# Optimization experiments

Measured on AMD Instinct MI355X. Metric: run time of the kernel, lower is better.

Reference implementation:

```python
import jax, jax.numpy as jnp
import numpy as np

# Model config (mirrors Mamba2Block(dim=256) with mamba_ssm defaults)
D_MODEL = 256
EXPAND = 2
D_INNER = D_MODEL * EXPAND          # 512
HEADDIM = D_MODEL * EXPAND // 8     # 64
NHEADS = D_INNER // HEADDIM         # 8
D_STATE = 64
D_CONV = 4
CONV_DIM = D_INNER + 2 * D_STATE    # 640 (ngroups=1)
D_IN_PROJ = 2 * D_INNER + 2 * D_STATE + NHEADS  # 1160
BATCH, SEQLEN = 2, 2048
EPS = 1e-5


def setup_inputs() -> dict:
    key = jax.random.key(0)
    ks = jax.random.split(key, 12)
    s = 0.02
    return {
        "hidden_states": jax.random.normal(ks[0], (BATCH, SEQLEN, D_MODEL), jnp.float32),
        "norm_w": jnp.ones((D_MODEL,), jnp.float32),
        "norm_b": jnp.zeros((D_MODEL,), jnp.float32),
        "W_in": jax.random.normal(ks[1], (D_MODEL, D_IN_PROJ), jnp.float32) * s,
        "conv_w": jax.random.normal(ks[2], (CONV_DIM, D_CONV), jnp.float32) * 0.25,
        "conv_b": jnp.zeros((CONV_DIM,), jnp.float32),
        "dt_bias": jax.random.uniform(ks[3], (NHEADS,), jnp.float32),
        "A_log": jax.random.uniform(ks[4], (NHEADS,), jnp.float32),  # A = -exp(A_log) in (-e, -1]
        "D_param": jnp.ones((NHEADS,), jnp.float32),
        "rms_w": jnp.ones((D_INNER,), jnp.float32),
        "W_out": jax.random.normal(ks[5], (D_INNER, D_MODEL), jnp.float32) * s,
    }


def _layer_norm(x, w, b):
    mu = jnp.mean(x, -1, keepdims=True)
    var = jnp.mean((x - mu) ** 2, -1, keepdims=True)
    return (x - mu) * jax.lax.rsqrt(var + EPS) * w + b


def _causal_depthwise_conv(x, w, b):
    # x: [B,L,C], w: [C,K] depthwise causal conv
    B, L, C = x.shape
    K = w.shape[1]
    xp = jnp.pad(x, ((0, 0), (K - 1, 0), (0, 0)))
    y = b
    for k in range(K):  # K=4, fixed small kernel
        y = y + w[:, k] * xp[:, k:k + L, :]
    return y


def reference(hidden_states, norm_w, norm_b, W_in, conv_w, conv_b, dt_bias, A_log, D_param, rms_w, W_out):
    B, L, D = hidden_states.shape
    residual = hidden_states                       # residual is None, drop_path=0
    x = _layer_norm(residual, norm_w, norm_b)      # pre-norm

    zxbcdt = jnp.einsum("bld,de->ble", x, W_in)    # [B,L,2*Di+2*N+H]
    z = zxbcdt[..., :D_INNER]
    xBC = zxbcdt[..., D_INNER:D_INNER + CONV_DIM]
    dt = zxbcdt[..., -NHEADS:]

    xBC = jax.nn.silu(_causal_depthwise_conv(xBC, conv_w, conv_b))
    xs = xBC[..., :D_INNER]
    Bm = xBC[..., D_INNER:D_INNER + D_STATE]       # [B,L,N] (ngroups=1)
    Cm = xBC[..., D_INNER + D_STATE:]              # [B,L,N]

    dt = jax.nn.softplus(dt + dt_bias)             # [B,L,H]
    A = -jnp.exp(A_log)                            # [H]
    dA = jnp.exp(dt * A)                           # [B,L,H]

    xh = xs.reshape(B, L, NHEADS, HEADDIM)         # [B,L,H,P]
    dtx = dt[..., None] * xh                       # [B,L,H,P]

    def step(s, inp):
        dA_t, dtx_t, B_t, C_t = inp                # [B,H],[B,H,P],[B,N],[B,N]
        s = s * dA_t[:, :, None, None] + dtx_t[..., None] * B_t[:, None, None, :]
        y_t = jnp.einsum("bhpn,bn->bhp", s, C_t)
        return s, y_t

    s0 = jnp.zeros((B, NHEADS, HEADDIM, D_STATE), hidden_states.dtype)
    xs_in = (jnp.swapaxes(dA, 0, 1), jnp.swapaxes(dtx, 0, 1),
             jnp.swapaxes(Bm, 0, 1), jnp.swapaxes(Cm, 0, 1))
    _, ys = jax.lax.scan(step, s0, xs_in)          # ys: [L,B,H,P]
    y = jnp.swapaxes(ys, 0, 1) + D_param[None, None, :, None] * xh  # skip term
    y = y.reshape(B, L, D_INNER)

    # gated RMSNorm (norm_before_gate=False): rmsnorm(y * silu(z)) * rms_w
    g = y * jax.nn.silu(z)
    g = g * jax.lax.rsqrt(jnp.mean(g * g, -1, keepdims=True) + EPS) * rms_w

    out = jnp.einsum("bld,de->ble", g, W_out)
    return out, residual
```

## Files before the change

kernel.cpp:

```cpp
#include <hip/hip_runtime.h>
#include <hip/hip_bf16.h>

#define BATCH 2
#define SEQLEN 2048
#define DMODEL 256
#define DINNER 512
#define NHEADS 8
#define HEADDIM 64
#define DSTATE 64
#define CONVDIM 640
#define DINPROJ 1160
#define NTOK (BATCH*SEQLEN)
#define Q 64
#define NCH (SEQLEN/Q)
#define NPAD2 1280
#define TS 72
#define RS3 196
#define GS 536

typedef short v8s __attribute__((ext_vector_type(8)));
typedef float v4f __attribute__((ext_vector_type(4)));

__device__ __forceinline__ unsigned short f2bf(float f){
    __hip_bfloat16 h = __float2bfloat16(f);
    return *reinterpret_cast<unsigned short*>(&h);
}
__device__ __forceinline__ float bf2f(unsigned short u){
    unsigned int x = ((unsigned int)u) << 16;
    return __uint_as_float(x);
}
__device__ __forceinline__ void gload_lds16(const unsigned short* g, unsigned short* l){
    __builtin_amdgcn_global_load_lds((const __attribute__((address_space(1))) void*)g,
                                     (__attribute__((address_space(3))) void*)l, 16, 0, 0);
}

__global__ __launch_bounds__(256) void k_prep(
        const float* __restrict__ hid, const float* __restrict__ nw, const float* __restrict__ nb,
        const float* __restrict__ Win, const float* __restrict__ Wout, const float* __restrict__ rms_w,
        float* __restrict__ res, unsigned short* __restrict__ Xb,
        unsigned short* __restrict__ Wti, unsigned short* __restrict__ Wto){
    int bx = blockIdx.x;
    int t = threadIdx.x;
    if(bx < 256){
        __shared__ float xs[16][DMODEL];
        int tok0 = bx*16;
        for(int i=0;i<16;i++){
            int idx = i*256+t; int j = idx>>8, c = idx&255;
            float v = hid[(size_t)(tok0+j)*DMODEL + c];
            xs[j][c] = v;
            res[(size_t)(tok0+j)*DMODEL + c] = v;
        }
        __syncthreads();
        int g = t>>4, il = t&15;
        float sum=0.f, sumsq=0.f;
        for(int i=0;i<16;i++){ float v = xs[g][il*16+i]; sum += v; sumsq += v*v; }
        #pragma unroll
        for(int m=1;m<16;m<<=1){ sum += __shfl_xor(sum,m); sumsq += __shfl_xor(sumsq,m); }
        float mu   = sum*(1.f/256.f);
        float var  = sumsq*(1.f/256.f) - mu*mu;
        float rstd = rsqrtf(var + 1e-5f);
        for(int i=0;i<16;i++){
            int c = il*16+i;
            xs[g][c] = (xs[g][c]-mu)*rstd*nw[c] + nb[c];
        }
        __syncthreads();
        for(int i=0;i<16;i++){
            int idx = i*256+t; int j = idx>>8, c = idx&255;
            Xb[(size_t)(tok0+j)*DMODEL + c] = f2bf(xs[j][c]);
        }
    } else if(bx < 256 + NPAD2/4){
        int n0 = (bx-256)*4, k = t;
        #pragma unroll
        for(int i=0;i<4;i++){
            int n = n0+i;
            float v = (n < DINPROJ) ? Win[(size_t)k*DINPROJ + n] : 0.f;
            Wti[(size_t)n*DMODEL + k] = f2bf(v);
        }
    } else {
        int n0 = (bx - 256 - NPAD2/4)*4;
        #pragma unroll
        for(int kk=0;kk<2;kk++){
            int k = t + kk*256;
            float rw = rms_w[k];
            #pragma unroll
            for(int i=0;i<4;i++){
                int n = n0+i;
                Wto[(size_t)n*DINNER + k] = f2bf(Wout[(size_t)k*DMODEL + n] * rw);
            }
        }
    }
}

__global__ __launch_bounds__(256) void k_gemm_in(
        const unsigned short* __restrict__ A, const unsigned short* __restrict__ Bt,
        unsigned short* __restrict__ zxb){
    __shared__ __align__(16) unsigned short As[128*32];
    __shared__ __align__(16) unsigned short Bs[128*32];
    int t = threadIdx.x;
    int lane = t & 63, w = t >> 6;
    int lanelow = lane & 15, quad = lane >> 4;
    int tok0 = blockIdx.x * 128;
    int n0   = blockIdx.y * 128;
    int rw = (w & 1) * 64, cw = (w >> 1) * 64;
    v4f acc[4][4];
    #pragma unroll
    for(int mi=0;mi<4;mi++)
        #pragma unroll
        for(int ni=0;ni<4;ni++)
            acc[mi][ni] = (v4f){0.f,0.f,0.f,0.f};
    for(int k0=0; k0<DMODEL; k0+=32){
        __syncthreads();
        #pragma unroll
        for(int cc=0; cc<2; cc++){
            int u = t + cc*256;
            int row = u>>2, off = u&3;
            int base_chunk = w*64 + cc*256;
            gload_lds16(A  + (size_t)(tok0+row)*DMODEL + k0 + off*8, &As[base_chunk*8]);
            gload_lds16(Bt + (size_t)(n0 +row)*DMODEL + k0 + off*8, &Bs[base_chunk*8]);
        }
        __syncthreads();
        v8s a[4], b[4];
        #pragma unroll
        for(int mi=0;mi<4;mi++) a[mi] = *(const v8s*)&As[(rw + mi*16 + lanelow)*32 + quad*8];
        #pragma unroll
        for(int ni=0;ni<4;ni++) b[ni] = *(const v8s*)&Bs[(cw + ni*16 + lanelow)*32 + quad*8];
        #pragma unroll
        for(int mi=0;mi<4;mi++)
            #pragma unroll
            for(int ni=0;ni<4;ni++)
                acc[mi][ni] = __builtin_amdgcn_mfma_f32_16x16x32_bf16(a[mi], b[ni], acc[mi][ni], 0,0,0);
    }
    #pragma unroll
    for(int mi=0;mi<4;mi++){
        #pragma unroll
        for(int ni=0;ni<4;ni++){
            int col = n0 + cw + ni*16 + lanelow;
            if(col < DINPROJ){
                #pragma unroll
                for(int r=0;r<4;r++){
                    int row = tok0 + rw + mi*16 + quad*4 + r;
                    zxb[(size_t)row*DINPROJ + col] = f2bf(acc[mi][ni][r]);
                }
            }
        }
    }
}

__global__ __launch_bounds__(256) void k_chunk1(
        const unsigned short* __restrict__ zxb, const float* __restrict__ conv_w, const float* __restrict__ conv_b,
        const float* __restrict__ dt_bias, const float* __restrict__ A_log, const float* __restrict__ D_param,
        unsigned short* __restrict__ yw16, unsigned short* __restrict__ contrib16,
        float* __restrict__ Larr, float* __restrict__ decayArr, unsigned short* __restrict__ Ccv){
    int blk = blockIdx.x;
    int c = blk & 31, h = (blk>>5)&7, b = blk>>8;
    int t = threadIdx.x;
    int lane = t & 63, w = t >> 6;
    int lanelow = lane & 15, quad = lane >> 4;
    __shared__ __align__(16) unsigned short Cb[64*TS];
    __shared__ __align__(16) unsigned short Bb[64*TS];
    __shared__ __align__(16) unsigned short BtW[64*TS];
    __shared__ __align__(16) unsigned short Xt[64*TS];
    __shared__ __align__(16) unsigned short GbufRaw[67*RS3];
    __shared__ float Ls[Q], dts[Q], wch[Q];
    unsigned short* raw  = GbufRaw;
    unsigned short* Gbuf = GbufRaw;
    int l0 = c*Q;
    int bh = b*NHEADS + h;
    const unsigned short* zbase = zxb + (size_t)(b*SEQLEN + l0)*DINPROJ;

    #pragma unroll
    for(int i=0;i<13;i++){
        int u = t + 256*i;
        if(u < 67*48){
            int row = u/48, seg = u - row*48;
            int l = l0 - 3 + row;
            int gcol = (seg<16) ? (DINNER + h*HEADDIM + seg*4) : (2*DINNER + (seg-16)*4);
            ushort4 v;
            if(l >= 0) v = *(const ushort4*)(zxb + ((size_t)b*SEQLEN + l)*DINPROJ + gcol);
            else { v.x=0; v.y=0; v.z=0; v.w=0; }
            *(ushort4*)&raw[row*RS3 + seg*4] = v;
        }
    }
    if(t < Q){
        float v = bf2f(zbase[(size_t)t*DINPROJ + (DINPROJ-NHEADS) + h]) + dt_bias[h];
        float dt = (v > 20.f) ? v : log1pf(__expf(v));
        float A  = -__expf(A_log[h]);
        float ld = dt*A;
        #pragma unroll
        for(int off=1; off<64; off<<=1){
            float u = __shfl_up(ld, off);
            if(lane >= off) ld += u;
        }
        Ls[t] = ld; dts[t] = dt;
    }
    __syncthreads();
    float L63 = Ls[Q-1];
    if(t < Q) wch[t] = __expf(L63 - Ls[t]) * dts[t];
    __syncthreads();

    unsigned short* CcP = Ccv + ((size_t)b*NCH + c)*4096;
    #pragma unroll
    for(int sblk=0; sblk<4; sblk++){
        #pragma unroll
        for(int i=0;i<3;i++){
            int u = t + 256*i;
            int stl = u & 15, grp = u >> 4;
            int st = sblk*16 + stl;
            int ch = grp*4;
            float xk[4][4];
            #pragma unroll
            for(int k=0;k<4;k++){
                ushort4 v = *(const ushort4*)&raw[(st+k)*RS3 + ch];
                xk[k][0]=bf2f(v.x); xk[k][1]=bf2f(v.y); xk[k][2]=bf2f(v.z); xk[k][3]=bf2f(v.w);
            }
            float wst = wch[st];
            #pragma unroll
            for(int j=0;j<4;j++){
                int chj = ch+j;
                int cc = (chj<64) ? (h*HEADDIM + chj) : (448 + chj);
                float4 wv = *(const float4*)&conv_w[cc*4];
                float acc = conv_b[cc] + wv.x*xk[0][j] + wv.y*xk[1][j] + wv.z*xk[2][j] + wv.w*xk[3][j];
                float sv = acc/(1.f+__expf(-acc));
                if(chj < 64){
                    Xt[chj*TS + st] = f2bf(sv);
                } else if(chj < 128){
                    int n = chj-64;
                    Bb[st*TS + n]  = f2bf(sv);
                    BtW[n*TS + st] = f2bf(sv*wst);
                } else {
                    int n = chj-128;
                    unsigned short sb16 = f2bf(sv);
                    Cb[st*TS + n] = sb16;
                    if(h==0) CcP[st*64 + n] = sb16;
                }
            }
        }
    }
    __syncthreads();
    v4f g[4];
    #pragma unroll
    for(int nt=0;nt<4;nt++) g[nt] = (v4f){0.f,0.f,0.f,0.f};
    #pragma unroll
    for(int kk=0;kk<2;kk++){
        v8s a = *(const v8s*)&Cb[(w*16+lanelow)*TS + kk*32 + quad*8];
        #pragma unroll
        for(int nt=0;nt<4;nt++){
            v8s bb = *(const v8s*)&Bb[(nt*16+lanelow)*TS + kk*32 + quad*8];
            g[nt] = __builtin_amdgcn_mfma_f32_16x16x32_bf16(a, bb, g[nt], 0,0,0);
        }
    }
    float Lrow[4];
    #pragma unroll
    for(int r=0;r<4;r++) Lrow[r] = Ls[w*16 + quad*4 + r];
    #pragma unroll
    for(int nt=0;nt<4;nt++){
        int col = nt*16 + lanelow;
        float Lc = Ls[col], dtc = dts[col];
        #pragma unroll
        for(int r=0;r<4;r++){
            int rowg = w*16 + quad*4 + r;
            float val = (col <= rowg) ? g[nt][r] * __expf(Lrow[r]-Lc) * dtc : 0.f;
            Gbuf[rowg*TS + col] = f2bf(val);
        }
    }
    __syncthreads();
    v4f ya[4], sa[4];
    #pragma unroll
    for(int nt=0;nt<4;nt++){ ya[nt]=(v4f){0.f,0.f,0.f,0.f}; sa[nt]=(v4f){0.f,0.f,0.f,0.f}; }
    #pragma unroll
    for(int kk=0;kk<2;kk++){
        v8s ag = *(const v8s*)&Gbuf[(w*16+lanelow)*TS + kk*32 + quad*8];
        v8s ax = *(const v8s*)&Xt[(w*16+lanelow)*TS + kk*32 + quad*8];
        #pragma unroll
        for(int nt=0;nt<4;nt++){
            v8s bx = *(const v8s*)&Xt[(nt*16+lanelow)*TS + kk*32 + quad*8];
            v8s bw = *(const v8s*)&BtW[(nt*16+lanelow)*TS + kk*32 + quad*8];
            ya[nt] = __builtin_amdgcn_mfma_f32_16x16x32_bf16(ag, bx, ya[nt], 0,0,0);
            sa[nt] = __builtin_amdgcn_mfma_f32_16x16x32_bf16(ax, bw, sa[nt], 0,0,0);
        }
    }
    float Dp = D_param[h];
    #pragma unroll
    for(int nt=0;nt<4;nt++){
        int col = nt*16 + lanelow;
        #pragma unroll
        for(int r=0;r<4;r++){
            int i = w*16 + quad*4 + r;
            float xval = bf2f(Xt[col*TS + i]);
            yw16[((size_t)b*SEQLEN + l0 + i)*DINNER + h*HEADDIM + col] = f2bf(ya[nt][r] + Dp*xval);
            contrib16[(((size_t)bh*NCH + c)*64 + i)*64 + col] = f2bf(sa[nt][r]);
        }
    }
    if(t < Q) Larr[((size_t)bh*NCH + c)*Q + t] = Ls[t];
    if(t == 0) decayArr[bh*NCH + c] = __expf(L63);
}

__global__ __launch_bounds__(256) void k_chunk2(const unsigned short* __restrict__ contrib16,
                                                const float* __restrict__ decayArr,
                                                unsigned short* __restrict__ Sb){
    int bh = blockIdx.x >> 4;
    int part = blockIdx.x & 15;
    int e = part*256 + threadIdx.x;
    const size_t base = (size_t)bh*NCH*4096 + e;
    float vals[NCH];
    #pragma unroll
    for(int c=0;c<NCH;c++) vals[c] = bf2f(contrib16[base + (size_t)c*4096]);
    float s = 0.f;
    #pragma unroll
    for(int c=0;c<NCH;c++){
        Sb[base + (size_t)c*4096] = f2bf(s);
        s = fmaf(s, decayArr[bh*NCH + c], vals[c]);
    }
}

__global__ __launch_bounds__(512) void k_tail(
        const unsigned short* __restrict__ Ccv, const unsigned short* __restrict__ Sb,
        const float* __restrict__ Larr, const unsigned short* __restrict__ yw16,
        const unsigned short* __restrict__ zxb, const unsigned short* __restrict__ Wto,
        float* __restrict__ out){
    int blk = blockIdx.x;
    int q4 = blk & 3, c = (blk>>2) & 31, b = blk >> 7;
    int t = threadIdx.x;
    int h = t >> 6, lane = t & 63;
    int lanelow = lane & 15, quad = lane >> 4;
    int bh = b*NHEADS + h;
    __shared__ __align__(16) unsigned short Gs[16*GS];
    __shared__ float wsum[8][16];
    __shared__ float rstdS[16];
    const unsigned short* Cp = Ccv + ((size_t)b*NCH + c)*4096;
    const unsigned short* Sp = Sb + ((size_t)bh*NCH + c)*4096;
    int row0 = q4*16;
    v8s a0 = *(const v8s*)(Cp + (row0+lanelow)*64 + quad*8);
    v8s a1 = *(const v8s*)(Cp + (row0+lanelow)*64 + 32 + quad*8);
    v8s s[4][2];
    #pragma unroll
    for(int nt=0;nt<4;nt++){
        s[nt][0] = *(const v8s*)(Sp + (nt*16+lanelow)*64 + quad*8);
        s[nt][1] = *(const v8s*)(Sp + (nt*16+lanelow)*64 + 32 + quad*8);
    }
    float sq[4] = {0.f,0.f,0.f,0.f};
    const float* Lp = Larr + ((size_t)bh*NCH + c)*Q;
    float eL[4];
    #pragma unroll
    for(int r=0;r<4;r++) eL[r] = __expf(Lp[row0 + quad*4 + r]);
    size_t tok0 = (size_t)b*SEQLEN + c*Q + row0;
    #pragma unroll
    for(int nt=0;nt<4;nt++){
        v4f acc = (v4f){0.f,0.f,0.f,0.f};
        acc = __builtin_amdgcn_mfma_f32_16x16x32_bf16(a0, s[nt][0], acc, 0,0,0);
        acc = __builtin_amdgcn_mfma_f32_16x16x32_bf16(a1, s[nt][1], acc, 0,0,0);
        int col = h*HEADDIM + nt*16 + lanelow;
        #pragma unroll
        for(int r=0;r<4;r++){
            size_t tok = tok0 + quad*4 + r;
            float yv = acc[r]*eL[r] + bf2f(yw16[tok*DINNER + col]);
            float z  = bf2f(zxb[tok*DINPROJ + col]);
            float gg = yv * (z/(1.f+__expf(-z)));
            Gs[(quad*4+r)*GS + col] = f2bf(gg);
            sq[r] += gg*gg;
        }
    }
    #pragma unroll
    for(int r=0;r<4;r++){
        float v = sq[r];
        #pragma unroll
        for(int m=1;m<16;m<<=1) v += __shfl_xor(v, m);
        sq[r] = v;
    }
    if(lanelow==0){
        #pragma unroll
        for(int r=0;r<4;r++) wsum[h][quad*4 + r] = sq[r];
    }
    __syncthreads();
    if(t < 16){
        float tot = 0.f;
        #pragma unroll
        for(int hh=0;hh<8;hh++) tot += wsum[hh][t];
        rstdS[t] = rsqrtf(tot*(1.f/512.f) + 1e-5f);
    }
    __syncthreads();
    v4f acc2[2];
    #pragma unroll
    for(int nt=0;nt<2;nt++) acc2[nt] = (v4f){0.f,0.f,0.f,0.f};
    for(int ki=0; ki<16; ki++){
        v8s a = *(const v8s*)&Gs[lanelow*GS + ki*32 + quad*8];
        #pragma unroll
        for(int nt=0;nt<2;nt++){
            v8s bfr = *(const v8s*)(Wto + (size_t)(h*32 + nt*16 + lanelow)*DINNER + ki*32 + quad*8);
            acc2[nt] = __builtin_amdgcn_mfma_f32_16x16x32_bf16(a, bfr, acc2[nt], 0,0,0);
        }
    }
    float rs[4];
    #pragma unroll
    for(int r=0;r<4;r++) rs[r] = rstdS[quad*4 + r];
    #pragma unroll
    for(int nt=0;nt<2;nt++){
        int col = h*32 + nt*16 + lanelow;
        #pragma unroll
        for(int r=0;r<4;r++)
            out[(tok0 + quad*4 + r)*DMODEL + col] = acc2[nt][r]*rs[r];
    }
}

extern "C" void kernel_launch(void* const* d_in, const int* in_sizes, int n_in,
                              void* d_out, int out_size, void* d_ws, size_t ws_size,
                              hipStream_t stream) {
    const float* hid     = (const float*)d_in[0];
    const float* norm_w  = (const float*)d_in[1];
    const float* norm_b  = (const float*)d_in[2];
    const float* Win     = (const float*)d_in[3];
    const float* conv_w  = (const float*)d_in[4];
    const float* conv_b  = (const float*)d_in[5];
    const float* dt_bias = (const float*)d_in[6];
    const float* A_log   = (const float*)d_in[7];
    const float* D_param = (const float*)d_in[8];
    const float* rms_w   = (const float*)d_in[9];
    const float* Wout    = (const float*)d_in[10];

    unsigned short* contrib16 = (unsigned short*)d_ws;
    float* Larr    = (float*)(contrib16 + (size_t)16*NCH*4096);
    float* decayA  = Larr + (size_t)16*NCH*Q;
    unsigned short* zxb  = (unsigned short*)(decayA + 512);
    unsigned short* yw16 = zxb + (size_t)NTOK*DINPROJ;
    unsigned short* Sb   = yw16 + (size_t)NTOK*DINNER;
    unsigned short* Ccv  = Sb + (size_t)16*NCH*4096;
    unsigned short* Xb   = Ccv + (size_t)BATCH*NCH*4096;
    unsigned short* Wti  = Xb + (size_t)NTOK*DMODEL;
    unsigned short* Wto  = Wti + (size_t)NPAD2*DMODEL;

    float* out = (float*)d_out;
    float* res = out + (size_t)NTOK*DMODEL;

    k_prep<<<256 + NPAD2/4 + DMODEL/4, 256, 0, stream>>>(hid, norm_w, norm_b, Win, Wout, rms_w, res, Xb, Wti, Wto);
    k_gemm_in<<<dim3(NTOK/128, NPAD2/128), 256, 0, stream>>>(Xb, Wti, zxb);
    k_chunk1<<<BATCH*NHEADS*NCH, 256, 0, stream>>>(zxb, conv_w, conv_b, dt_bias, A_log, D_param,
                                                   yw16, contrib16, Larr, decayA, Ccv);
    k_chunk2<<<256, 256, 0, stream>>>(contrib16, decayA, Sb);
    k_tail<<<BATCH*NCH*4, 512, 0, stream>>>(Ccv, Sb, Larr, yw16, zxb, Wto, out);
}
```

Before: 129.3 us.

## Retile input GEMM to 64x64 full-K tiles and double-buffer conv staging in chunk1

The input projection GEMM moves from 128x128 tiles with a K loop of 32 to 64x64 tiles that load the whole K=256 slab into LDS once, with an XOR swizzle to avoid bank conflicts. This gives four times as many blocks for occupancy and removes the per-step barriers. In k_chunk1 the 67-row raw staging buffer becomes a double-buffered 19-row window: the next 16-step slab is loaded into registers while the current one is convolved, and the redundant barrier around the wch computation is removed using a shuffle. In exchange, the GEMM uses more LDS per block and each B tile is reused less.

```diff
diff --git a/kernel.cpp b/kernel.cpp
--- a/kernel.cpp
+++ b/kernel.cpp
@@ -94,46 +94,52 @@
 __global__ __launch_bounds__(256) void k_gemm_in(
         const unsigned short* __restrict__ A, const unsigned short* __restrict__ Bt,
         unsigned short* __restrict__ zxb){
-    __shared__ __align__(16) unsigned short As[128*32];
-    __shared__ __align__(16) unsigned short Bs[128*32];
+    __shared__ __align__(16) unsigned short As[64*256];
+    __shared__ __align__(16) unsigned short Bs[64*256];
     int t = threadIdx.x;
     int lane = t & 63, w = t >> 6;
     int lanelow = lane & 15, quad = lane >> 4;
-    int tok0 = blockIdx.x * 128;
-    int n0   = blockIdx.y * 128;
-    int rw = (w & 1) * 64, cw = (w >> 1) * 64;
-    v4f acc[4][4];
-    #pragma unroll
-    for(int mi=0;mi<4;mi++)
-        #pragma unroll
-        for(int ni=0;ni<4;ni++)
+    int tok0 = blockIdx.x * 64;
+    int n0   = blockIdx.y * 64;
+    int rw = (w & 1) * 32, cw = (w >> 1) * 32;
+    #pragma unroll
+    for(int k=0;k<8;k++){
+        int u = t + k*256;
+        int row = u >> 5, off = u & 31;
+        int soff = off ^ (row & 7);
+        gload_lds16(A  + (size_t)(tok0+row)*DMODEL + soff*8, &As[(w*64 + k*256)*8]);
+        gload_lds16(Bt + (size_t)(n0 +row)*DMODEL + soff*8, &Bs[(w*64 + k*256)*8]);
+    }
+    __syncthreads();
+    v4f acc[2][2];
+    #pragma unroll
+    for(int mi=0;mi<2;mi++)
+        #pragma unroll
+        for(int ni=0;ni<2;ni++)
             acc[mi][ni] = (v4f){0.f,0.f,0.f,0.f};
-    for(int k0=0; k0<DMODEL; k0+=32){
-        __syncthreads();
-        #pragma unroll
-        for(int cc=0; cc<2; cc++){
-            int u = t + cc*256;
-            int row = u>>2, off = u&3;
-            int base_chunk = w*64 + cc*256;
-            gload_lds16(A  + (size_t)(tok0+row)*DMODEL + k0 + off*8, &As[base_chunk*8]);
-            gload_lds16(Bt + (size_t)(n0 +row)*DMODEL + k0 + off*8, &Bs[base_chunk*8]);
-        }
-        __syncthreads();
-        v8s a[4], b[4];
-        #pragma unroll
-        for(int mi=0;mi<4;mi++) a[mi] = *(const v8s*)&As[(rw + mi*16 + lanelow)*32 + quad*8];
-        #pragma unroll
-        for(int ni=0;ni<4;ni++) b[ni] = *(const v8s*)&Bs[(cw + ni*16 + lanelow)*32 + quad*8];
-        #pragma unroll
-        for(int mi=0;mi<4;mi++)
-            #pragma unroll
-            for(int ni=0;ni<4;ni++)
+    #pragma unroll
+    for(int k0=0;k0<8;k0++){
+        v8s a[2], b[2];
+        #pragma unroll
+        for(int mi=0;mi<2;mi++){
+            int r = rw + mi*16 + lanelow;
+            a[mi] = *(const v8s*)&As[r*256 + (((k0*4 + quad) ^ (r & 7)))*8];
+        }
+        #pragma unroll
+        for(int ni=0;ni<2;ni++){
+            int r = cw + ni*16 + lanelow;
+            b[ni] = *(const v8s*)&Bs[r*256 + (((k0*4 + quad) ^ (r & 7)))*8];
+        }
+        #pragma unroll
+        for(int mi=0;mi<2;mi++)
+            #pragma unroll
+            for(int ni=0;ni<2;ni++)
                 acc[mi][ni] = __builtin_amdgcn_mfma_f32_16x16x32_bf16(a[mi], b[ni], acc[mi][ni], 0,0,0);
     }
     #pragma unroll
-    for(int mi=0;mi<4;mi++){
-        #pragma unroll
-        for(int ni=0;ni<4;ni++){
+    for(int mi=0;mi<2;mi++){
+        #pragma unroll
+        for(int ni=0;ni<2;ni++){
             int col = n0 + cw + ni*16 + lanelow;
             if(col < DINPROJ){
                 #pragma unroll
@@ -160,25 +166,27 @@
     __shared__ __align__(16) unsigned short Bb[64*TS];
     __shared__ __align__(16) unsigned short BtW[64*TS];
     __shared__ __align__(16) unsigned short Xt[64*TS];
-    __shared__ __align__(16) unsigned short GbufRaw[67*RS3];
+    __shared__ __align__(16) unsigned short BufRegion[2*19*RS3];
     __shared__ float Ls[Q], dts[Q], wch[Q];
-    unsigned short* raw  = GbufRaw;
-    unsigned short* Gbuf = GbufRaw;
+    unsigned short* Gbuf = BufRegion;
     int l0 = c*Q;
     int bh = b*NHEADS + h;
     const unsigned short* zbase = zxb + (size_t)(b*SEQLEN + l0)*DINPROJ;
 
-    #pragma unroll
-    for(int i=0;i<13;i++){
-        int u = t + 256*i;
-        if(u < 67*48){
-            int row = u/48, seg = u - row*48;
-            int l = l0 - 3 + row;
-            int gcol = (seg<16) ? (DINNER + h*HEADDIM + seg*4) : (2*DINNER + (seg-16)*4);
-            ushort4 v;
-            if(l >= 0) v = *(const ushort4*)(zxb + ((size_t)b*SEQLEN + l)*DINPROJ + gcol);
-            else { v.x=0; v.y=0; v.z=0; v.w=0; }
-            *(ushort4*)&raw[row*RS3 + seg*4] = v;
+    {
+        unsigned short* buf = BufRegion;
+        #pragma unroll
+        for(int i=0;i<4;i++){
+            int u = t + 256*i;
+            if(u < 19*48){
+                int row = u/48, seg = u - row*48;
+                int l = l0 - 3 + row;
+                int gcol = (seg<16) ? (DINNER + h*HEADDIM + seg*4) : (2*DINNER + (seg-16)*4);
+                ushort4 v;
+                if(l >= 0) v = *(const ushort4*)(zxb + ((size_t)b*SEQLEN + l)*DINPROJ + gcol);
+                else { v.x=0; v.y=0; v.z=0; v.w=0; }
+                *(ushort4*)&buf[row*RS3 + seg*4] = v;
+            }
         }
     }
     if(t < Q){
@@ -192,25 +200,38 @@
             if(lane >= off) ld += u;
         }
         Ls[t] = ld; dts[t] = dt;
+        float l63 = __shfl(ld, 63);
+        wch[t] = __expf(l63 - ld) * dt;
     }
     __syncthreads();
-    float L63 = Ls[Q-1];
-    if(t < Q) wch[t] = __expf(L63 - Ls[t]) * dts[t];
-    __syncthreads();
 
     unsigned short* CcP = Ccv + ((size_t)b*NCH + c)*4096;
-    #pragma unroll
-    for(int sblk=0; sblk<4; sblk++){
+    for(int s=0; s<4; s++){
+        unsigned short* cur = BufRegion + (s&1)*(19*RS3);
+        unsigned short* nxt = BufRegion + ((s+1)&1)*(19*RS3);
+        ushort4 stg[4];
+        if(s < 3){
+            #pragma unroll
+            for(int i=0;i<4;i++){
+                int u = t + 256*i;
+                if(u < 19*48){
+                    int row = u/48, seg = u - row*48;
+                    int l = l0 + (s+1)*16 - 3 + row;
+                    int gcol = (seg<16) ? (DINNER + h*HEADDIM + seg*4) : (2*DINNER + (seg-16)*4);
+                    stg[i] = *(const ushort4*)(zxb + ((size_t)b*SEQLEN + l)*DINPROJ + gcol);
+                }
+            }
+        }
         #pragma unroll
         for(int i=0;i<3;i++){
             int u = t + 256*i;
             int stl = u & 15, grp = u >> 4;
-            int st = sblk*16 + stl;
+            int st = s*16 + stl;
             int ch = grp*4;
             float xk[4][4];
             #pragma unroll
             for(int k=0;k<4;k++){
-                ushort4 v = *(const ushort4*)&raw[(st+k)*RS3 + ch];
+                ushort4 v = *(const ushort4*)&cur[(stl+k)*RS3 + ch];
                 xk[k][0]=bf2f(v.x); xk[k][1]=bf2f(v.y); xk[k][2]=bf2f(v.z); xk[k][3]=bf2f(v.w);
             }
             float wst = wch[st];
@@ -235,8 +256,18 @@
                 }
             }
         }
-    }
-    __syncthreads();
+        if(s < 3){
+            #pragma unroll
+            for(int i=0;i<4;i++){
+                int u = t + 256*i;
+                if(u < 19*48){
+                    int row = u/48, seg = u - row*48;
+                    *(ushort4*)&nxt[row*RS3 + seg*4] = stg[i];
+                }
+            }
+        }
+        __syncthreads();
+    }
     v4f g[4];
     #pragma unroll
     for(int nt=0;nt<4;nt++) g[nt] = (v4f){0.f,0.f,0.f,0.f};
@@ -292,7 +323,7 @@
         }
     }
     if(t < Q) Larr[((size_t)bh*NCH + c)*Q + t] = Ls[t];
-    if(t == 0) decayArr[bh*NCH + c] = __expf(L63);
+    if(t == 0) decayArr[bh*NCH + c] = __expf(Ls[Q-1]);
 }
 
 __global__ __launch_bounds__(256) void k_chunk2(const unsigned short* __restrict__ contrib16,
@@ -432,7 +463,7 @@
     float* res = out + (size_t)NTOK*DMODEL;
 
     k_prep<<<256 + NPAD2/4 + DMODEL/4, 256, 0, stream>>>(hid, norm_w, norm_b, Win, Wout, rms_w, res, Xb, Wti, Wto);
-    k_gemm_in<<<dim3(NTOK/128, NPAD2/128), 256, 0, stream>>>(Xb, Wti, zxb);
+    k_gemm_in<<<dim3(NTOK/64, NPAD2/64), 256, 0, stream>>>(Xb, Wti, zxb);
     k_chunk1<<<BATCH*NHEADS*NCH, 256, 0, stream>>>(zxb, conv_w, conv_b, dt_bias, A_log, D_param,
                                                    yw16, contrib16, Larr, decayA, Ccv);
     k_chunk2<<<256, 256, 0, stream>>>(contrib16, decayA, Sb);
```

Measured after the change: 123.8 us. 1.04x faster.
